# Kernel optimization log

Measured on AMD Instinct MI355X. Metric: run time of the kernel, lower is better.

Reference implementation:

```python
import jax, jax.numpy as jnp
import numpy as np
from jax import lax

NKP = 21  # hand keypoints
CH = 32   # channel width forced by K.dot(g, W) with W:[input_ch, output_dim]
OUT_DIM = 32


def setup_inputs() -> dict:
    key = jax.random.key(0)
    ks = jax.random.split(key, 9)
    B, H, W = 8, 96, 96
    s = 0.05
    return {
        "x": jax.random.normal(ks[0], (B, H, W, CH), dtype=jnp.float32),
        # shared 1x1 conv (conv2): 1x1 conv == matmul over channels
        "w2": jax.random.normal(ks[1], (CH, CH), dtype=jnp.float32) * s,
        "b2": jnp.zeros((CH,), dtype=jnp.float32),
        # per-keypoint effective 1x1 conv (conv2a over concat of identical f blocks
        # collapses exactly to a 32->32 kernel = sum of per-block slices)
        "wa": jax.random.normal(ks[2], (NKP, CH, CH), dtype=jnp.float32) * s,
        "ba": jnp.zeros((NKP, CH), dtype=jnp.float32),
        # per-keypoint 3x3 conv (conv2b), HWIO layout
        "wb": jax.random.normal(ks[3], (NKP, 3, 3, CH, CH), dtype=jnp.float32) * s,
        "bb": jnp.zeros((NKP, CH), dtype=jnp.float32),
        # per-keypoint learned projection W_i : [CH, output_dim]
        "Wp": jax.random.normal(ks[4], (NKP, CH, OUT_DIM), dtype=jnp.float32) * s,
    }


def _conv3x3(h, w, b):
    # h: [B,H,W,C], w: [3,3,C,C]
    y = lax.conv_general_dilated(h, w, (1, 1), "SAME",
                                 dimension_numbers=("NHWC", "HWIO", "NHWC"))
    return jax.nn.relu(y + b)


def reference(x, w2, b2, wa, ba, wb, bb, Wp):
    f = jax.nn.relu(jnp.einsum("bhwc,cd->bhwd", x, w2) + b2)          # [B,H,W,32]
    # per-keypoint 1x1 conv on concat([f, f_j...]) == effective 32->32 1x1 conv
    h = jax.nn.relu(jnp.einsum("bhwc,ncd->nbhwd", f, wa)
                    + ba[:, None, None, None, :])                      # [21,B,H,W,32]
    g = jax.vmap(_conv3x3)(h, wb, bb)                                  # [21,B,H,W,32]
    # sum over output_dim of (g @ W_i) == g @ W_i.sum(-1)
    lsum = jnp.einsum("nbhwc,nc->nbhw", g, Wp.sum(axis=-1))            # [21,B,H,W]
    fn = f.sum(axis=-1)[None] + lsum                                   # [21,B,H,W]
    return jnp.moveaxis(fn, 0, -1)                                     # [B,H,W,21]
```

## Files before the change

kernel.cpp:

```cpp
#include <hip/hip_runtime.h>

#define BATCH 8
#define IMH 96
#define IMW 96
#define CH 32
#define NKP 21
#define TILE 16
#define HALO 18
#define FPITCH 40
#define NPIX 324
#define NPIX_PAD 336
#define NGRP 3
#define FBLK 1152

typedef __bf16 bf16x8 __attribute__((ext_vector_type(8)));
typedef __bf16 bf16x4 __attribute__((ext_vector_type(4)));
typedef float  f32x4  __attribute__((ext_vector_type(4)));

static __device__ inline f32x4 mfma16(bf16x8 a, bf16x8 b, f32x4 c) {
    return __builtin_amdgcn_mfma_f32_16x16x32_bf16(a, b, c, 0, 0, 0);
}

__global__ void __launch_bounds__(64)
prep_kernel(const float* __restrict__ x,
            const float* __restrict__ w2, const float* __restrict__ b2,
            const float* __restrict__ wa, const float* __restrict__ wb,
            const float* __restrict__ Wp,
            __bf16* __restrict__ fout, float* __restrict__ fsum_out,
            __bf16* __restrict__ wfrag, float* __restrict__ wv)
{
    const int bx = blockIdx.x;
    const int lane = threadIdx.x;
    if (bx < FBLK) {
        const int gp = bx * 64 + lane;
        const float* xp = x + (size_t)gp * CH;
        float xv[CH];
        #pragma unroll
        for (int e = 0; e < CH; e += 4) {
            float4 v = *(const float4*)(xp + e);
            xv[e] = v.x; xv[e+1] = v.y; xv[e+2] = v.z; xv[e+3] = v.w;
        }
        float f[CH];
        #pragma unroll
        for (int c = 0; c < CH; ++c) f[c] = b2[c];
        #pragma unroll
        for (int e = 0; e < CH; ++e) {
            const float xe = xv[e];
            const float* wr = w2 + e * CH;
            #pragma unroll
            for (int c = 0; c < CH; ++c) f[c] = fmaf(xe, wr[c], f[c]);
        }
        float fs = 0.f;
        #pragma unroll
        for (int c = 0; c < CH; ++c) { f[c] = fmaxf(f[c], 0.f); fs += f[c]; }
        #pragma unroll
        for (int q = 0; q < 4; ++q) {
            bf16x8 v;
            #pragma unroll
            for (int j = 0; j < 8; ++j) v[j] = (__bf16)f[q * 8 + j];
            *(bf16x8*)&fout[(size_t)gp * CH + q * 8] = v;
        }
        fsum_out[gp] = fs;
    } else {
        const int n = bx - FBLK;
        const int r4 = lane & 15, kb = (lane >> 4) * 8;
        const float* wan = wa + n * CH * CH;
        #pragma unroll
        for (int hf = 0; hf < 2; ++hf) {
            bf16x8 v;
            #pragma unroll
            for (int j = 0; j < 8; ++j)
                v[j] = (__bf16)wan[(kb + j) * CH + hf * 16 + r4];
            *(bf16x8*)&wfrag[(((size_t)n * 20 + hf) * 64 + lane) * 8] = v;
        }
        const float* wbn = wb + (size_t)n * 9 * CH * CH;
        for (int t = 0; t < 9; ++t)
            #pragma unroll
            for (int hf = 0; hf < 2; ++hf) {
                bf16x8 v;
                #pragma unroll
                for (int j = 0; j < 8; ++j)
                    v[j] = (__bf16)wbn[(t * CH + kb + j) * CH + hf * 16 + r4];
                *(bf16x8*)&wfrag[(((size_t)n * 20 + 2 + t * 2 + hf) * 64 + lane) * 8] = v;
            }
        if (lane < CH) {
            const float* wp = Wp + (n * CH + lane) * CH;
            float s = 0.f;
            #pragma unroll
            for (int d = 0; d < CH; ++d) s += wp[d];
            wv[n * CH + lane] = s;
        }
    }
}

__global__ void __launch_bounds__(256, 4)
ckp_mfma4_kernel(const __bf16* __restrict__ fws, const float* __restrict__ fsum_ws,
                 const __bf16* __restrict__ wfrag, const float* __restrict__ wvws,
                 const float* __restrict__ ba, const float* __restrict__ bb,
                 float* __restrict__ out)
{
    __shared__ __bf16 sH[NPIX_PAD * FPITCH];

    const int tid  = threadIdx.x;
    const int tile = blockIdx.x;
    const int b    = blockIdx.y;
    const int ty0  = (tile / (IMW / TILE)) * TILE;
    const int tx0  = (tile % (IMW / TILE)) * TILE;

    const int lane = tid & 63;
    const int w    = tid >> 6;
    const int r4   = lane & 15;
    const int g16  = lane >> 4;
    const int kb   = g16 * 8;
    const int kb4  = g16 * 4;
    const int w4   = w * 4;

    int voff[6]; unsigned dmask = 0;
    #pragma unroll
    for (int i = 0; i < 6; ++i) {
        const int t  = w + 4 * i;
        const int p  = t * 16 + r4;
        const int hy = p / HALO, hx = p % HALO;
        const int Y  = ty0 + hy - 1, X = tx0 + hx - 1;
        const bool dv = (t <= 20) & (hy < HALO) & (Y >= 0) & (Y < IMH) & (X >= 0) & (X < IMW);
        const int Yc = min(max(Y, 0), IMH - 1), Xc = min(max(X, 0), IMW - 1);
        voff[i] = ((b * IMH + Yc) * IMW + Xc) * CH + kb;
        dmask |= (dv ? 1u : 0u) << i;
    }

    for (int ni = 0; ni < NGRP; ++ni) {
        const int n = blockIdx.z * NGRP + ni;
        const __bf16* wf = wfrag + (size_t)n * 20 * 64 * 8;
        bf16x8 wafr0 = *(const bf16x8*)&wf[((size_t)0 * 64 + lane) * 8];
        bf16x8 wafr1 = *(const bf16x8*)&wf[((size_t)1 * 64 + lane) * 8];
        const f32x4 ba0 = *(const f32x4*)&ba[n * CH + kb4];
        const f32x4 ba1 = *(const f32x4*)&ba[n * CH + 16 + kb4];

        if (ni) __syncthreads();

        #pragma unroll
        for (int i = 0; i < 6; ++i) {
            const int t = w + 4 * i;
            if (t <= 20) {
                bf16x8 v = *(const bf16x8*)&fws[voff[i]];
                const bool dv = (dmask >> i) & 1;
                if (!dv) {
                    #pragma unroll
                    for (int j = 0; j < 8; ++j) v[j] = (__bf16)0.f;
                }
                const f32x4 z = {0.f, 0.f, 0.f, 0.f};
                f32x4 a0 = mfma16(wafr0, v, z);
                f32x4 a1 = mfma16(wafr1, v, z);
                const int p = t * 16 + r4;
                bf16x4 h0, h1;
                #pragma unroll
                for (int r = 0; r < 4; ++r) {
                    h0[r] = dv ? (__bf16)fmaxf(a0[r] + ba0[r], 0.f) : (__bf16)0.f;
                    h1[r] = dv ? (__bf16)fmaxf(a1[r] + ba1[r], 0.f) : (__bf16)0.f;
                }
                *(bf16x4*)&sH[p * FPITCH + kb4]      = h0;
                *(bf16x4*)&sH[p * FPITCH + 16 + kb4] = h1;
            }
        }
        __syncthreads();

        f32x4 acc[4][2];
        #pragma unroll
        for (int ai = 0; ai < 4; ++ai) {
            acc[ai][0] = (f32x4){0.f, 0.f, 0.f, 0.f};
            acc[ai][1] = (f32x4){0.f, 0.f, 0.f, 0.f};
        }
        #pragma unroll
        for (int dx = 0; dx < 3; ++dx) {
            bf16x8 wt[3][2];
            #pragma unroll
            for (int dy = 0; dy < 3; ++dy)
                #pragma unroll
                for (int hf = 0; hf < 2; ++hf)
                    wt[dy][hf] = *(const bf16x8*)&wf[((size_t)(2 + (dy * 3 + dx) * 2 + hf) * 64 + lane) * 8];
            #pragma unroll
            for (int k = 0; k < 6; ++k) {
                bf16x8 hfr = *(const bf16x8*)&sH[((w4 + k) * HALO + r4 + dx) * FPITCH + kb];
                #pragma unroll
                for (int dy = 0; dy < 3; ++dy) {
                    const int ai = k - dy;
                    if (ai >= 0 && ai < 4) {
                        acc[ai][0] = mfma16(wt[dy][0], hfr, acc[ai][0]);
                        acc[ai][1] = mfma16(wt[dy][1], hfr, acc[ai][1]);
                    }
                }
            }
        }

        const f32x4 bb0 = *(const f32x4*)&bb[n * CH + kb4];
        const f32x4 bb1 = *(const f32x4*)&bb[n * CH + 16 + kb4];
        const f32x4 wv0 = *(const f32x4*)&wvws[n * CH + kb4];
        const f32x4 wv1 = *(const f32x4*)&wvws[n * CH + 16 + kb4];
        #pragma unroll
        for (int ai = 0; ai < 4; ++ai) {
            float s = 0.f;
            #pragma unroll
            for (int r = 0; r < 4; ++r) {
                s += fmaxf(acc[ai][0][r] + bb0[r], 0.f) * wv0[r];
                s += fmaxf(acc[ai][1][r] + bb1[r], 0.f) * wv1[r];
            }
            s += __shfl_xor(s, 16);
            s += __shfl_xor(s, 32);
            if (g16 == 0) {
                const int gp = (b * IMH + ty0 + w4 + ai) * IMW + tx0 + r4;
                out[(size_t)gp * NKP + n] = s + fsum_ws[gp];
            }
        }
    }
}

#define PITCH 33
__global__ void __launch_bounds__(256)
ckp_fused_kernel(const float* __restrict__ x,
                 const float* __restrict__ w2, const float* __restrict__ b2,
                 const float* __restrict__ wa, const float* __restrict__ ba,
                 const float* __restrict__ wb, const float* __restrict__ bb,
                 const float* __restrict__ Wp,
                 float* __restrict__ out)
{
    __shared__ float sH[HALO * HALO * PITCH];
    __shared__ float sFsum[TILE * TILE];
    __shared__ float sWv[CH];

    const int tid  = threadIdx.x;
    const int tile = blockIdx.x;
    const int b    = blockIdx.y;
    const int n    = blockIdx.z;
    const int ty0  = (tile / (IMW / TILE)) * TILE;
    const int tx0  = (tile % (IMW / TILE)) * TILE;

    if (tid < CH) {
        const float* wp = Wp + (n * CH + tid) * CH;
        float s = 0.f;
        #pragma unroll
        for (int d = 0; d < CH; ++d) s += wp[d];
        sWv[tid] = s;
    }
    const float* wan = wa + n * CH * CH;
    const float* ban = ba + n * CH;

    for (int p = tid; p < HALO * HALO; p += 256) {
        const int hy = p / HALO, hx = p % HALO;
        const int Y = ty0 + hy - 1, X = tx0 + hx - 1;
        float* dst = &sH[p * PITCH];
        if (Y >= 0 && Y < IMH && X >= 0 && X < IMW) {
            const float* xp = x + (((size_t)b * IMH + Y) * IMW + X) * CH;
            float xv[CH];
            #pragma unroll
            for (int e = 0; e < CH; e += 4) {
                float4 v = *(const float4*)(xp + e);
                xv[e] = v.x; xv[e+1] = v.y; xv[e+2] = v.z; xv[e+3] = v.w;
            }
            float f[CH];
            #pragma unroll
            for (int c = 0; c < CH; ++c) f[c] = b2[c];
            #pragma unroll
            for (int e = 0; e < CH; ++e) {
                const float xe = xv[e];
                const float* wr = w2 + e * CH;
                #pragma unroll
                for (int c = 0; c < CH; ++c) f[c] = fmaf(xe, wr[c], f[c]);
            }
            float fs = 0.f;
            #pragma unroll
            for (int c = 0; c < CH; ++c) { f[c] = fmaxf(f[c], 0.f); fs += f[c]; }
            if (hy >= 1 && hy <= TILE && hx >= 1 && hx <= TILE)
                sFsum[(hy - 1) * TILE + (hx - 1)] = fs;
            float h[CH];
            #pragma unroll
            for (int c = 0; c < CH; ++c) h[c] = ban[c];
            #pragma unroll
            for (int e = 0; e < CH; ++e) {
                const float fe = f[e];
                const float* wr = wan + e * CH;
                #pragma unroll
                for (int c = 0; c < CH; ++c) h[c] = fmaf(fe, wr[c], h[c]);
            }
            #pragma unroll
            for (int c = 0; c < CH; ++c) dst[c] = fmaxf(h[c], 0.f);
        } else {
            #pragma unroll
            for (int c = 0; c < CH; ++c) dst[c] = 0.f;
        }
    }
    __syncthreads();

    const int iy = tid / TILE, ix = tid % TILE;
    const float* wbn = wb + n * 9 * CH * CH;
    const float* bbn = bb + n * CH;
    float g[CH];
    #pragma unroll
    for (int c = 0; c < CH; ++c) g[c] = bbn[c];
    for (int dy = 0; dy < 3; ++dy) {
        for (int dx = 0; dx < 3; ++dx) {
            const float* hrow = &sH[((iy + dy) * HALO + (ix + dx)) * PITCH];
            const float* wr0 = wbn + (dy * 3 + dx) * CH * CH;
            #pragma unroll
            for (int e = 0; e < CH; ++e) {
                const float hv = hrow[e];
                const float* wr = wr0 + e * CH;
                #pragma unroll
                for (int c = 0; c < CH; ++c) g[c] = fmaf(hv, wr[c], g[c]);
            }
        }
    }
    float lsum = 0.f;
    #pragma unroll
    for (int c = 0; c < CH; ++c) lsum = fmaf(fmaxf(g[c], 0.f), sWv[c], lsum);
    const int Y = ty0 + iy, X = tx0 + ix;
    out[(((size_t)b * IMH + Y) * IMW + X) * NKP + n] = sFsum[tid] + lsum;
}

extern "C" void kernel_launch(void* const* d_in, const int* in_sizes, int n_in,
                              void* d_out, int out_size, void* d_ws, size_t ws_size,
                              hipStream_t stream) {
    const float* x  = (const float*)d_in[0];
    const float* w2 = (const float*)d_in[1];
    const float* b2 = (const float*)d_in[2];
    const float* wa = (const float*)d_in[3];
    const float* ba = (const float*)d_in[4];
    const float* wb = (const float*)d_in[5];
    const float* bb = (const float*)d_in[6];
    const float* Wp = (const float*)d_in[7];
    float* out = (float*)d_out;

    const size_t npix     = (size_t)BATCH * IMH * IMW;
    const size_t f_bytes  = npix * CH * sizeof(__bf16);
    const size_t fs_bytes = npix * sizeof(float);
    const size_t wf_bytes = (size_t)NKP * 20 * 64 * 8 * sizeof(__bf16);
    const size_t wv_bytes = (size_t)NKP * CH * sizeof(float);
    const size_t need = f_bytes + fs_bytes + wf_bytes + wv_bytes;

    if (ws_size >= need) {
        __bf16* f_ws    = (__bf16*)d_ws;
        float*  fsum_ws = (float*)((char*)d_ws + f_bytes);
        __bf16* wf_ws   = (__bf16*)((char*)d_ws + f_bytes + fs_bytes);
        float*  wv_ws   = (float*)((char*)d_ws + f_bytes + fs_bytes + wf_bytes);

        prep_kernel<<<dim3(FBLK + NKP), dim3(64), 0, stream>>>(
            x, w2, b2, wa, wb, Wp, f_ws, fsum_ws, wf_ws, wv_ws);
        dim3 grid((IMH / TILE) * (IMW / TILE), BATCH, NKP / NGRP);
        ckp_mfma4_kernel<<<grid, dim3(256), 0, stream>>>(f_ws, fsum_ws, wf_ws, wv_ws, ba, bb, out);
    } else {
        dim3 grid((IMH / TILE) * (IMW / TILE), BATCH, NKP);
        ckp_fused_kernel<<<grid, dim3(256), 0, stream>>>(x, w2, b2, wa, ba, wb, bb, Wp, out);
    }
}
```

Before: 54.42 us.

## Assign one keypoint per block and loop over two tiles with register-resident weights

The main conv kernel now gives each block a single keypoint and walks two spatial tiles, instead of one tile and three keypoints. All 3x3 weight fragments and biases are loaded into registers once per block, and the feature loads for a tile are issued together before the MFMA stage. This cuts repeated weight fetches and makes loads more independent, but it raises register pressure, so launch bounds drop to 3 blocks per CU. The grid becomes 18x8x21 blocks.

After: 89.41 us. 64.3% more time.

```diff
diff --git a/kernel.cpp b/kernel.cpp
--- a/kernel.cpp
+++ b/kernel.cpp
@@ -10,8 +10,8 @@
 #define FPITCH 40
 #define NPIX 324
 #define NPIX_PAD 336
-#define NGRP 3
 #define FBLK 1152
+#define NTP 2
 
 typedef __bf16 bf16x8 __attribute__((ext_vector_type(8)));
 typedef __bf16 bf16x4 __attribute__((ext_vector_type(4)));
@@ -93,19 +93,18 @@
     }
 }
 
-__global__ void __launch_bounds__(256, 4)
-ckp_mfma4_kernel(const __bf16* __restrict__ fws, const float* __restrict__ fsum_ws,
+__global__ void __launch_bounds__(256, 3)
+ckp_mfma5_kernel(const __bf16* __restrict__ fws, const float* __restrict__ fsum_ws,
                  const __bf16* __restrict__ wfrag, const float* __restrict__ wvws,
                  const float* __restrict__ ba, const float* __restrict__ bb,
                  float* __restrict__ out)
 {
     __shared__ __bf16 sH[NPIX_PAD * FPITCH];
 
-    const int tid  = threadIdx.x;
-    const int tile = blockIdx.x;
-    const int b    = blockIdx.y;
-    const int ty0  = (tile / (IMW / TILE)) * TILE;
-    const int tx0  = (tile % (IMW / TILE)) * TILE;
+    const int tid = threadIdx.x;
+    const int gx  = blockIdx.x;
+    const int b   = blockIdx.y;
+    const int n   = blockIdx.z;
 
     const int lane = tid & 63;
     const int w    = tid >> 6;
@@ -115,34 +114,51 @@
     const int kb4  = g16 * 4;
     const int w4   = w * 4;
 
-    int voff[6]; unsigned dmask = 0;
+    const __bf16* wf = wfrag + (size_t)n * 20 * 64 * 8;
+    const bf16x8 wafr0 = *(const bf16x8*)&wf[((size_t)0 * 64 + lane) * 8];
+    const bf16x8 wafr1 = *(const bf16x8*)&wf[((size_t)1 * 64 + lane) * 8];
+    bf16x8 wtfr[9][2];
     #pragma unroll
-    for (int i = 0; i < 6; ++i) {
-        const int t  = w + 4 * i;
-        const int p  = t * 16 + r4;
-        const int hy = p / HALO, hx = p % HALO;
-        const int Y  = ty0 + hy - 1, X = tx0 + hx - 1;
-        const bool dv = (t <= 20) & (hy < HALO) & (Y >= 0) & (Y < IMH) & (X >= 0) & (X < IMW);
-        const int Yc = min(max(Y, 0), IMH - 1), Xc = min(max(X, 0), IMW - 1);
-        voff[i] = ((b * IMH + Yc) * IMW + Xc) * CH + kb;
-        dmask |= (dv ? 1u : 0u) << i;
-    }
-
-    for (int ni = 0; ni < NGRP; ++ni) {
-        const int n = blockIdx.z * NGRP + ni;
-        const __bf16* wf = wfrag + (size_t)n * 20 * 64 * 8;
-        bf16x8 wafr0 = *(const bf16x8*)&wf[((size_t)0 * 64 + lane) * 8];
-        bf16x8 wafr1 = *(const bf16x8*)&wf[((size_t)1 * 64 + lane) * 8];
-        const f32x4 ba0 = *(const f32x4*)&ba[n * CH + kb4];
-        const f32x4 ba1 = *(const f32x4*)&ba[n * CH + 16 + kb4];
-
-        if (ni) __syncthreads();
-
+    for (int t = 0; t < 9; ++t)
+        #pragma unroll
+        for (int hf = 0; hf < 2; ++hf)
+            wtfr[t][hf] = *(const bf16x8*)&wf[((size_t)(2 + t * 2 + hf) * 64 + lane) * 8];
+    const f32x4 ba0 = *(const f32x4*)&ba[n * CH + kb4];
+    const f32x4 ba1 = *(const f32x4*)&ba[n * CH + 16 + kb4];
+    const f32x4 bb0 = *(const f32x4*)&bb[n * CH + kb4];
+    const f32x4 bb1 = *(const f32x4*)&bb[n * CH + 16 + kb4];
+    const f32x4 wv0 = *(const f32x4*)&wvws[n * CH + kb4];
+    const f32x4 wv1 = *(const f32x4*)&wvws[n * CH + 16 + kb4];
+
+    for (int tp = 0; tp < NTP; ++tp) {
+        const int tile = gx * NTP + tp;
+        const int ty0  = (tile / (IMW / TILE)) * TILE;
+        const int tx0  = (tile % (IMW / TILE)) * TILE;
+
+        int voff[6]; unsigned dmask = 0;
+        #pragma unroll
+        for (int i = 0; i < 6; ++i) {
+            const int t  = w + 4 * i;
+            const int p  = t * 16 + r4;
+            const int hy = p / HALO, hx = p % HALO;
+            const int Y  = ty0 + hy - 1, X = tx0 + hx - 1;
+            const bool dv = (t <= 20) & (hy < HALO) & (Y >= 0) & (Y < IMH) & (X >= 0) & (X < IMW);
+            const int Yc = min(max(Y, 0), IMH - 1), Xc = min(max(X, 0), IMW - 1);
+            voff[i] = ((b * IMH + Yc) * IMW + Xc) * CH + kb;
+            dmask |= (dv ? 1u : 0u) << i;
+        }
+
+        if (tp) __syncthreads();
+
+        bf16x8 fv[6];
+        #pragma unroll
+        for (int i = 0; i < 6; ++i)
+            fv[i] = *(const bf16x8*)&fws[voff[i]];
         #pragma unroll
         for (int i = 0; i < 6; ++i) {
             const int t = w + 4 * i;
             if (t <= 20) {
-                bf16x8 v = *(const bf16x8*)&fws[voff[i]];
+                bf16x8 v = fv[i];
                 const bool dv = (dmask >> i) & 1;
                 if (!dv) {
                     #pragma unroll
@@ -172,12 +188,6 @@
         }
         #pragma unroll
         for (int dx = 0; dx < 3; ++dx) {
-            bf16x8 wt[3][2];
-            #pragma unroll
-            for (int dy = 0; dy < 3; ++dy)
-                #pragma unroll
-                for (int hf = 0; hf < 2; ++hf)
-                    wt[dy][hf] = *(const bf16x8*)&wf[((size_t)(2 + (dy * 3 + dx) * 2 + hf) * 64 + lane) * 8];
             #pragma unroll
             for (int k = 0; k < 6; ++k) {
                 bf16x8 hfr = *(const bf16x8*)&sH[((w4 + k) * HALO + r4 + dx) * FPITCH + kb];
@@ -185,17 +195,13 @@
                 for (int dy = 0; dy < 3; ++dy) {
                     const int ai = k - dy;
                     if (ai >= 0 && ai < 4) {
-                        acc[ai][0] = mfma16(wt[dy][0], hfr, acc[ai][0]);
-                        acc[ai][1] = mfma16(wt[dy][1], hfr, acc[ai][1]);
+                        acc[ai][0] = mfma16(wtfr[dy * 3 + dx][0], hfr, acc[ai][0]);
+                        acc[ai][1] = mfma16(wtfr[dy * 3 + dx][1], hfr, acc[ai][1]);
                     }
                 }
             }
         }
 
-        const f32x4 bb0 = *(const f32x4*)&bb[n * CH + kb4];
-        const f32x4 bb1 = *(const f32x4*)&bb[n * CH + 16 + kb4];
-        const f32x4 wv0 = *(const f32x4*)&wvws[n * CH + kb4];
-        const f32x4 wv1 = *(const f32x4*)&wvws[n * CH + 16 + kb4];
         #pragma unroll
         for (int ai = 0; ai < 4; ++ai) {
             float s = 0.f;
@@ -344,8 +350,8 @@
 
         prep_kernel<<<dim3(FBLK + NKP), dim3(64), 0, stream>>>(
             x, w2, b2, wa, wb, Wp, f_ws, fsum_ws, wf_ws, wv_ws);
-        dim3 grid((IMH / TILE) * (IMW / TILE), BATCH, NKP / NGRP);
-        ckp_mfma4_kernel<<<grid, dim3(256), 0, stream>>>(f_ws, fsum_ws, wf_ws, wv_ws, ba, bb, out);
+        dim3 grid((IMH / TILE) * (IMW / TILE) / NTP, BATCH, NKP);
+        ckp_mfma5_kernel<<<grid, dim3(256), 0, stream>>>(f_ws, fsum_ws, wf_ws, wv_ws, ba, bb, out);
     } else {
         dim3 grid((IMH / TILE) * (IMW / TILE), BATCH, NKP);
         ckp_fused_kernel<<<grid, dim3(256), 0, stream>>>(x, w2, b2, wa, ba, wb, bb, Wp, out);
```

## Software-pipeline keypoint loop with double-buffered LDS and hoisted feature loads

Applied to the files above, without the earlier changes.

Restructures the per-keypoint loop into a skewed software pipeline. The 1x1 conv for keypoint n+1 writes into one of two LDS buffers while the 3x3 conv for keypoint n reads the other, which cuts one barrier per iteration. The halo feature vectors and fsum values are now loaded once into registers before the loop rather than reloaded for every keypoint, and the biases are folded into the MFMA accumulator init. In exchange, LDS use doubles and register pressure rises, so the occupancy hint drops from 4 to 2 blocks per CU.

New measurement: 55.65 us. 2.3% more time.

```diff
diff --git a/kernel.cpp b/kernel.cpp
--- a/kernel.cpp
+++ b/kernel.cpp
@@ -93,19 +93,20 @@
     }
 }
 
-__global__ void __launch_bounds__(256, 4)
-ckp_mfma4_kernel(const __bf16* __restrict__ fws, const float* __restrict__ fsum_ws,
+__global__ void __launch_bounds__(256, 2)
+ckp_mfma6_kernel(const __bf16* __restrict__ fws, const float* __restrict__ fsum_ws,
                  const __bf16* __restrict__ wfrag, const float* __restrict__ wvws,
                  const float* __restrict__ ba, const float* __restrict__ bb,
                  float* __restrict__ out)
 {
-    __shared__ __bf16 sH[NPIX_PAD * FPITCH];
-
-    const int tid  = threadIdx.x;
-    const int tile = blockIdx.x;
-    const int b    = blockIdx.y;
-    const int ty0  = (tile / (IMW / TILE)) * TILE;
-    const int tx0  = (tile % (IMW / TILE)) * TILE;
+    __shared__ __bf16 sH[2][NPIX_PAD * FPITCH];
+
+    const int tid   = threadIdx.x;
+    const int tile  = blockIdx.x;
+    const int b     = blockIdx.y;
+    const int nbase = blockIdx.z * NGRP;
+    const int ty0   = (tile / (IMW / TILE)) * TILE;
+    const int tx0   = (tile % (IMW / TILE)) * TILE;
 
     const int lane = tid & 63;
     const int w    = tid >> 6;
@@ -115,7 +116,7 @@
     const int kb4  = g16 * 4;
     const int w4   = w * 4;
 
-    int voff[6]; unsigned dmask = 0;
+    bf16x8 fv[6]; unsigned dmask = 0;
     #pragma unroll
     for (int i = 0; i < 6; ++i) {
         const int t  = w + 4 * i;
@@ -124,93 +125,103 @@
         const int Y  = ty0 + hy - 1, X = tx0 + hx - 1;
         const bool dv = (t <= 20) & (hy < HALO) & (Y >= 0) & (Y < IMH) & (X >= 0) & (X < IMW);
         const int Yc = min(max(Y, 0), IMH - 1), Xc = min(max(X, 0), IMW - 1);
-        voff[i] = ((b * IMH + Yc) * IMW + Xc) * CH + kb;
+        bf16x8 v = *(const bf16x8*)&fws[((b * IMH + Yc) * IMW + Xc) * CH + kb];
+        if (!dv) {
+            #pragma unroll
+            for (int j = 0; j < 8; ++j) v[j] = (__bf16)0.f;
+        }
+        fv[i] = v;
         dmask |= (dv ? 1u : 0u) << i;
     }
-
-    for (int ni = 0; ni < NGRP; ++ni) {
-        const int n = blockIdx.z * NGRP + ni;
-        const __bf16* wf = wfrag + (size_t)n * 20 * 64 * 8;
-        bf16x8 wafr0 = *(const bf16x8*)&wf[((size_t)0 * 64 + lane) * 8];
-        bf16x8 wafr1 = *(const bf16x8*)&wf[((size_t)1 * 64 + lane) * 8];
-        const f32x4 ba0 = *(const f32x4*)&ba[n * CH + kb4];
-        const f32x4 ba1 = *(const f32x4*)&ba[n * CH + 16 + kb4];
-
-        if (ni) __syncthreads();
-
-        #pragma unroll
-        for (int i = 0; i < 6; ++i) {
-            const int t = w + 4 * i;
-            if (t <= 20) {
-                bf16x8 v = *(const bf16x8*)&fws[voff[i]];
-                const bool dv = (dmask >> i) & 1;
-                if (!dv) {
+    float fs4[4];
+    #pragma unroll
+    for (int ai = 0; ai < 4; ++ai)
+        fs4[ai] = fsum_ws[(b * IMH + ty0 + w4 + ai) * IMW + tx0 + r4];
+
+    #pragma unroll
+    for (int ni = 0; ni <= NGRP; ++ni) {
+        if (ni < NGRP) {
+            const int n = nbase + ni;
+            const __bf16* wf = wfrag + (size_t)n * 20 * 64 * 8;
+            const bf16x8 wafr0 = *(const bf16x8*)&wf[((size_t)0 * 64 + lane) * 8];
+            const bf16x8 wafr1 = *(const bf16x8*)&wf[((size_t)1 * 64 + lane) * 8];
+            const f32x4 ba0 = *(const f32x4*)&ba[n * CH + kb4];
+            const f32x4 ba1 = *(const f32x4*)&ba[n * CH + 16 + kb4];
+            __bf16* sb = &sH[ni & 1][0];
+            #pragma unroll
+            for (int i = 0; i < 6; ++i) {
+                const int t = w + 4 * i;
+                if (t <= 20) {
+                    f32x4 a0 = mfma16(wafr0, fv[i], ba0);
+                    f32x4 a1 = mfma16(wafr1, fv[i], ba1);
+                    const int p = t * 16 + r4;
+                    const bool dv = (dmask >> i) & 1;
+                    bf16x4 h0, h1;
                     #pragma unroll
-                    for (int j = 0; j < 8; ++j) v[j] = (__bf16)0.f;
+                    for (int r = 0; r < 4; ++r) {
+                        h0[r] = dv ? (__bf16)fmaxf(a0[r], 0.f) : (__bf16)0.f;
+                        h1[r] = dv ? (__bf16)fmaxf(a1[r], 0.f) : (__bf16)0.f;
+                    }
+                    *(bf16x4*)&sb[p * FPITCH + kb4]      = h0;
+                    *(bf16x4*)&sb[p * FPITCH + 16 + kb4] = h1;
                 }
-                const f32x4 z = {0.f, 0.f, 0.f, 0.f};
-                f32x4 a0 = mfma16(wafr0, v, z);
-                f32x4 a1 = mfma16(wafr1, v, z);
-                const int p = t * 16 + r4;
-                bf16x4 h0, h1;
-                #pragma unroll
-                for (int r = 0; r < 4; ++r) {
-                    h0[r] = dv ? (__bf16)fmaxf(a0[r] + ba0[r], 0.f) : (__bf16)0.f;
-                    h1[r] = dv ? (__bf16)fmaxf(a1[r] + ba1[r], 0.f) : (__bf16)0.f;
-                }
-                *(bf16x4*)&sH[p * FPITCH + kb4]      = h0;
-                *(bf16x4*)&sH[p * FPITCH + 16 + kb4] = h1;
-            }
-        }
-        __syncthreads();
-
-        f32x4 acc[4][2];
-        #pragma unroll
-        for (int ai = 0; ai < 4; ++ai) {
-            acc[ai][0] = (f32x4){0.f, 0.f, 0.f, 0.f};
-            acc[ai][1] = (f32x4){0.f, 0.f, 0.f, 0.f};
-        }
-        #pragma unroll
-        for (int dx = 0; dx < 3; ++dx) {
-            bf16x8 wt[3][2];
-            #pragma unroll
-            for (int dy = 0; dy < 3; ++dy)
-                #pragma unroll
-                for (int hf = 0; hf < 2; ++hf)
-                    wt[dy][hf] = *(const bf16x8*)&wf[((size_t)(2 + (dy * 3 + dx) * 2 + hf) * 64 + lane) * 8];
-            #pragma unroll
-            for (int k = 0; k < 6; ++k) {
-                bf16x8 hfr = *(const bf16x8*)&sH[((w4 + k) * HALO + r4 + dx) * FPITCH + kb];
-                #pragma unroll
-                for (int dy = 0; dy < 3; ++dy) {
-                    const int ai = k - dy;
-                    if (ai >= 0 && ai < 4) {
-                        acc[ai][0] = mfma16(wt[dy][0], hfr, acc[ai][0]);
-                        acc[ai][1] = mfma16(wt[dy][1], hfr, acc[ai][1]);
+            }
+        }
+
+        if (ni > 0) {
+            const int n = nbase + ni - 1;
+            const __bf16* wf = wfrag + (size_t)n * 20 * 64 * 8;
+            const f32x4 bb0 = *(const f32x4*)&bb[n * CH + kb4];
+            const f32x4 bb1 = *(const f32x4*)&bb[n * CH + 16 + kb4];
+            const f32x4 wv0 = *(const f32x4*)&wvws[n * CH + kb4];
+            const f32x4 wv1 = *(const f32x4*)&wvws[n * CH + 16 + kb4];
+            const __bf16* sb = &sH[(ni - 1) & 1][0];
+
+            f32x4 acc[4][2];
+            #pragma unroll
+            for (int ai = 0; ai < 4; ++ai) {
+                acc[ai][0] = bb0;
+                acc[ai][1] = bb1;
+            }
+            #pragma unroll
+            for (int dx = 0; dx < 3; ++dx) {
+                bf16x8 wt[3][2];
+                #pragma unroll
+                for (int dy = 0; dy < 3; ++dy)
+                    #pragma unroll
+                    for (int hf = 0; hf < 2; ++hf)
+                        wt[dy][hf] = *(const bf16x8*)&wf[((size_t)(2 + (dy * 3 + dx) * 2 + hf) * 64 + lane) * 8];
+                #pragma unroll
+                for (int k = 0; k < 6; ++k) {
+                    bf16x8 hfr = *(const bf16x8*)&sb[((w4 + k) * HALO + r4 + dx) * FPITCH + kb];
+                    #pragma unroll
+                    for (int dy = 0; dy < 3; ++dy) {
+                        const int ai = k - dy;
+                        if (ai >= 0 && ai < 4) {
+                            acc[ai][0] = mfma16(wt[dy][0], hfr, acc[ai][0]);
+                            acc[ai][1] = mfma16(wt[dy][1], hfr, acc[ai][1]);
+                        }
                     }
                 }
             }
-        }
-
-        const f32x4 bb0 = *(const f32x4*)&bb[n * CH + kb4];
-        const f32x4 bb1 = *(const f32x4*)&bb[n * CH + 16 + kb4];
-        const f32x4 wv0 = *(const f32x4*)&wvws[n * CH + kb4];
-        const f32x4 wv1 = *(const f32x4*)&wvws[n * CH + 16 + kb4];
-        #pragma unroll
-        for (int ai = 0; ai < 4; ++ai) {
-            float s = 0.f;
-            #pragma unroll
-            for (int r = 0; r < 4; ++r) {
-                s += fmaxf(acc[ai][0][r] + bb0[r], 0.f) * wv0[r];
-                s += fmaxf(acc[ai][1][r] + bb1[r], 0.f) * wv1[r];
-            }
-            s += __shfl_xor(s, 16);
-            s += __shfl_xor(s, 32);
-            if (g16 == 0) {
-                const int gp = (b * IMH + ty0 + w4 + ai) * IMW + tx0 + r4;
-                out[(size_t)gp * NKP + n] = s + fsum_ws[gp];
-            }
-        }
+            #pragma unroll
+            for (int ai = 0; ai < 4; ++ai) {
+                float s = 0.f;
+                #pragma unroll
+                for (int r = 0; r < 4; ++r) {
+                    s += fmaxf(acc[ai][0][r], 0.f) * wv0[r];
+                    s += fmaxf(acc[ai][1][r], 0.f) * wv1[r];
+                }
+                s += __shfl_xor(s, 16);
+                s += __shfl_xor(s, 32);
+                if (g16 == 0) {
+                    const int gp = (b * IMH + ty0 + w4 + ai) * IMW + tx0 + r4;
+                    out[(size_t)gp * NKP + n] = s + fs4[ai];
+                }
+            }
+        }
+
+        if (ni < NGRP) __syncthreads();
     }
 }
 
@@ -345,7 +356,7 @@
         prep_kernel<<<dim3(FBLK + NKP), dim3(64), 0, stream>>>(
             x, w2, b2, wa, wb, Wp, f_ws, fsum_ws, wf_ws, wv_ws);
         dim3 grid((IMH / TILE) * (IMW / TILE), BATCH, NKP / NGRP);
-        ckp_mfma4_kernel<<<grid, dim3(256), 0, stream>>>(f_ws, fsum_ws, wf_ws, wv_ws, ba, bb, out);
+        ckp_mfma6_kernel<<<grid, dim3(256), 0, stream>>>(f_ws, fsum_ws, wf_ws, wv_ws, ba, bb, out);
     } else {
         dim3 grid((IMH / TILE) * (IMW / TILE), BATCH, NKP);
         ckp_fused_kernel<<<grid, dim3(256), 0, stream>>>(x, w2, b2, wa, ba, wb, bb, Wp, out);
```

## Switch conv kernel to 32x32x16 MFMA with 32x8 tiles and folded biases

Applied to the files above, without the earlier changes.

Replaces the 16x16x32 bf16 MFMA path with 32x32x16 MFMA and rebuilds the weight fragment layout in the prep kernel to match. The spatial tile changes from 16x16 to 32-wide by 8-tall, so each wave covers two full 32-pixel rows with a 34x10 halo. Biases are now loaded as accumulator fragments, removing separate bias adds, and the reduction shuffles drop from two to one. The goal is fewer MFMA issues and less LDS and shuffle traffic per output. The cost is a larger halo overhead per tile and a different LDS access pattern that could cause bank conflicts.

Measured after the change: 63.53 us (median of 2 runs). 16.7% more time.

```diff
diff --git a/kernel.cpp b/kernel.cpp
--- a/kernel.cpp
+++ b/kernel.cpp
@@ -5,20 +5,24 @@
 #define IMW 96
 #define CH 32
 #define NKP 21
-#define TILE 16
-#define HALO 18
+#define TW 32
+#define TH 8
+#define HW 34
+#define HH 10
+#define NPIXH 340
+#define NSTRIP 11
+#define NSLOT 352
 #define FPITCH 40
-#define NPIX 324
-#define NPIX_PAD 336
 #define NGRP 3
 #define FBLK 1152
 
 typedef __bf16 bf16x8 __attribute__((ext_vector_type(8)));
 typedef __bf16 bf16x4 __attribute__((ext_vector_type(4)));
 typedef float  f32x4  __attribute__((ext_vector_type(4)));
-
-static __device__ inline f32x4 mfma16(bf16x8 a, bf16x8 b, f32x4 c) {
-    return __builtin_amdgcn_mfma_f32_16x16x32_bf16(a, b, c, 0, 0, 0);
+typedef float  f32x16 __attribute__((ext_vector_type(16)));
+
+static __device__ inline f32x16 mfma32(bf16x8 a, bf16x8 b, f32x16 c) {
+    return __builtin_amdgcn_mfma_f32_32x32x16_bf16(a, b, c, 0, 0, 0);
 }
 
 __global__ void __launch_bounds__(64)
@@ -63,25 +67,25 @@
         fsum_out[gp] = fs;
     } else {
         const int n = bx - FBLK;
-        const int r4 = lane & 15, kb = (lane >> 4) * 8;
+        const int m = lane & 31, hi = lane >> 5;
         const float* wan = wa + n * CH * CH;
         #pragma unroll
-        for (int hf = 0; hf < 2; ++hf) {
+        for (int kh = 0; kh < 2; ++kh) {
             bf16x8 v;
             #pragma unroll
             for (int j = 0; j < 8; ++j)
-                v[j] = (__bf16)wan[(kb + j) * CH + hf * 16 + r4];
-            *(bf16x8*)&wfrag[(((size_t)n * 20 + hf) * 64 + lane) * 8] = v;
+                v[j] = (__bf16)wan[(kh * 16 + hi * 8 + j) * CH + m];
+            *(bf16x8*)&wfrag[(((size_t)n * 20 + kh) * 64 + lane) * 8] = v;
         }
         const float* wbn = wb + (size_t)n * 9 * CH * CH;
         for (int t = 0; t < 9; ++t)
             #pragma unroll
-            for (int hf = 0; hf < 2; ++hf) {
+            for (int kh = 0; kh < 2; ++kh) {
                 bf16x8 v;
                 #pragma unroll
                 for (int j = 0; j < 8; ++j)
-                    v[j] = (__bf16)wbn[(t * CH + kb + j) * CH + hf * 16 + r4];
-                *(bf16x8*)&wfrag[(((size_t)n * 20 + 2 + t * 2 + hf) * 64 + lane) * 8] = v;
+                    v[j] = (__bf16)wbn[(t * CH + kh * 16 + hi * 8 + j) * CH + m];
+                *(bf16x8*)&wfrag[(((size_t)n * 20 + 2 + t * 2 + kh) * 64 + lane) * 8] = v;
             }
         if (lane < CH) {
             const float* wp = Wp + (n * CH + lane) * CH;
@@ -93,128 +97,142 @@
     }
 }
 
+static __device__ inline f32x16 load_cfrag(const float* p, int hi) {
+    f32x16 out;
+    #pragma unroll
+    for (int q = 0; q < 4; ++q) {
+        f32x4 v = *(const f32x4*)&p[q * 8 + hi * 4];
+        #pragma unroll
+        for (int r = 0; r < 4; ++r) out[q * 4 + r] = v[r];
+    }
+    return out;
+}
+
 __global__ void __launch_bounds__(256, 4)
-ckp_mfma4_kernel(const __bf16* __restrict__ fws, const float* __restrict__ fsum_ws,
+ckp_mfma7_kernel(const __bf16* __restrict__ fws, const float* __restrict__ fsum_ws,
                  const __bf16* __restrict__ wfrag, const float* __restrict__ wvws,
                  const float* __restrict__ ba, const float* __restrict__ bb,
                  float* __restrict__ out)
 {
-    __shared__ __bf16 sH[NPIX_PAD * FPITCH];
-
-    const int tid  = threadIdx.x;
-    const int tile = blockIdx.x;
-    const int b    = blockIdx.y;
-    const int ty0  = (tile / (IMW / TILE)) * TILE;
-    const int tx0  = (tile % (IMW / TILE)) * TILE;
+    __shared__ __bf16 sH[NSLOT * FPITCH];
+
+    const int tid   = threadIdx.x;
+    const int tile  = blockIdx.x;
+    const int b     = blockIdx.y;
+    const int nbase = blockIdx.z * NGRP;
+    const int ty0   = (tile % (IMH / TH)) * TH;
+    const int tx0   = (tile / (IMH / TH)) * TW;
 
     const int lane = tid & 63;
     const int w    = tid >> 6;
-    const int r4   = lane & 15;
-    const int g16  = lane >> 4;
-    const int kb   = g16 * 8;
-    const int kb4  = g16 * 4;
-    const int w4   = w * 4;
-
-    int voff[6]; unsigned dmask = 0;
-    #pragma unroll
-    for (int i = 0; i < 6; ++i) {
+    const int c5   = lane & 31;
+    const int hi   = lane >> 5;
+    const int w2r  = w * 2;
+
+    int voff[3]; unsigned dmask = 0;
+    #pragma unroll
+    for (int i = 0; i < 3; ++i) {
         const int t  = w + 4 * i;
-        const int p  = t * 16 + r4;
-        const int hy = p / HALO, hx = p % HALO;
+        const int px = t * 32 + c5;
+        const int hy = px / HW, hx = px % HW;
         const int Y  = ty0 + hy - 1, X = tx0 + hx - 1;
-        const bool dv = (t <= 20) & (hy < HALO) & (Y >= 0) & (Y < IMH) & (X >= 0) & (X < IMW);
+        const bool dv = (px < NPIXH) & (Y >= 0) & (Y < IMH) & (X >= 0) & (X < IMW);
         const int Yc = min(max(Y, 0), IMH - 1), Xc = min(max(X, 0), IMW - 1);
-        voff[i] = ((b * IMH + Yc) * IMW + Xc) * CH + kb;
+        voff[i] = ((b * IMH + Yc) * IMW + Xc) * CH + hi * 8;
         dmask |= (dv ? 1u : 0u) << i;
     }
+    int wo[3];
+    #pragma unroll
+    for (int i = 0; i < 3; ++i) wo[i] = ((w + 4 * i) * 32 + c5) * FPITCH + 4 * hi;
+    int ro[4];
+    #pragma unroll
+    for (int h4 = 0; h4 < 4; ++h4) ro[h4] = ((w2r + h4) * HW + c5) * FPITCH + 8 * hi;
+    float fs2[2];
+    #pragma unroll
+    for (int ri = 0; ri < 2; ++ri)
+        fs2[ri] = fsum_ws[(b * IMH + ty0 + w2r + ri) * IMW + tx0 + c5];
 
     for (int ni = 0; ni < NGRP; ++ni) {
-        const int n = blockIdx.z * NGRP + ni;
+        const int n = nbase + ni;
         const __bf16* wf = wfrag + (size_t)n * 20 * 64 * 8;
-        bf16x8 wafr0 = *(const bf16x8*)&wf[((size_t)0 * 64 + lane) * 8];
-        bf16x8 wafr1 = *(const bf16x8*)&wf[((size_t)1 * 64 + lane) * 8];
-        const f32x4 ba0 = *(const f32x4*)&ba[n * CH + kb4];
-        const f32x4 ba1 = *(const f32x4*)&ba[n * CH + 16 + kb4];
+        const bf16x8 wa0 = *(const bf16x8*)&wf[((size_t)0 * 64 + lane) * 8];
+        const bf16x8 wa1 = *(const bf16x8*)&wf[((size_t)1 * 64 + lane) * 8];
+        const f32x16 baf = load_cfrag(ba + n * CH, hi);
 
         if (ni) __syncthreads();
 
         #pragma unroll
-        for (int i = 0; i < 6; ++i) {
+        for (int i = 0; i < 3; ++i) {
             const int t = w + 4 * i;
-            if (t <= 20) {
-                bf16x8 v = *(const bf16x8*)&fws[voff[i]];
+            if (t < NSTRIP) {
+                bf16x8 f0 = *(const bf16x8*)&fws[voff[i]];
+                bf16x8 f1 = *(const bf16x8*)&fws[voff[i] + 16];
+                f32x16 a = mfma32(wa0, f0, baf);
+                a = mfma32(wa1, f1, a);
                 const bool dv = (dmask >> i) & 1;
-                if (!dv) {
+                #pragma unroll
+                for (int q = 0; q < 4; ++q) {
+                    bf16x4 hq;
                     #pragma unroll
-                    for (int j = 0; j < 8; ++j) v[j] = (__bf16)0.f;
+                    for (int r = 0; r < 4; ++r)
+                        hq[r] = dv ? (__bf16)fmaxf(a[q * 4 + r], 0.f) : (__bf16)0.f;
+                    *(bf16x4*)&sH[wo[i] + 8 * q] = hq;
                 }
-                const f32x4 z = {0.f, 0.f, 0.f, 0.f};
-                f32x4 a0 = mfma16(wafr0, v, z);
-                f32x4 a1 = mfma16(wafr1, v, z);
-                const int p = t * 16 + r4;
-                bf16x4 h0, h1;
-                #pragma unroll
-                for (int r = 0; r < 4; ++r) {
-                    h0[r] = dv ? (__bf16)fmaxf(a0[r] + ba0[r], 0.f) : (__bf16)0.f;
-                    h1[r] = dv ? (__bf16)fmaxf(a1[r] + ba1[r], 0.f) : (__bf16)0.f;
-                }
-                *(bf16x4*)&sH[p * FPITCH + kb4]      = h0;
-                *(bf16x4*)&sH[p * FPITCH + 16 + kb4] = h1;
             }
         }
         __syncthreads();
 
-        f32x4 acc[4][2];
-        #pragma unroll
-        for (int ai = 0; ai < 4; ++ai) {
-            acc[ai][0] = (f32x4){0.f, 0.f, 0.f, 0.f};
-            acc[ai][1] = (f32x4){0.f, 0.f, 0.f, 0.f};
-        }
+        const f32x16 bbf = load_cfrag(bb + n * CH, hi);
+        f32x16 acc0, acc1;
         #pragma unroll
         for (int dx = 0; dx < 3; ++dx) {
             bf16x8 wt[3][2];
             #pragma unroll
             for (int dy = 0; dy < 3; ++dy)
                 #pragma unroll
-                for (int hf = 0; hf < 2; ++hf)
-                    wt[dy][hf] = *(const bf16x8*)&wf[((size_t)(2 + (dy * 3 + dx) * 2 + hf) * 64 + lane) * 8];
-            #pragma unroll
-            for (int k = 0; k < 6; ++k) {
-                bf16x8 hfr = *(const bf16x8*)&sH[((w4 + k) * HALO + r4 + dx) * FPITCH + kb];
+                for (int kh = 0; kh < 2; ++kh)
+                    wt[dy][kh] = *(const bf16x8*)&wf[((size_t)(2 + (dy * 3 + dx) * 2 + kh) * 64 + lane) * 8];
+            #pragma unroll
+            for (int h4 = 0; h4 < 4; ++h4) {
+                const int ad = ro[h4] + dx * FPITCH;
+                bf16x8 B0 = *(const bf16x8*)&sH[ad];
+                bf16x8 B1 = *(const bf16x8*)&sH[ad + 16];
                 #pragma unroll
                 for (int dy = 0; dy < 3; ++dy) {
-                    const int ai = k - dy;
-                    if (ai >= 0 && ai < 4) {
-                        acc[ai][0] = mfma16(wt[dy][0], hfr, acc[ai][0]);
-                        acc[ai][1] = mfma16(wt[dy][1], hfr, acc[ai][1]);
+                    const int ri = h4 - dy;
+                    if (ri == 0) {
+                        const bool first = (dx == 0 && dy == 0);
+                        acc0 = mfma32(wt[dy][0], B0, first ? bbf : acc0);
+                        acc0 = mfma32(wt[dy][1], B1, acc0);
+                    } else if (ri == 1) {
+                        const bool first = (dx == 0 && dy == 0);
+                        acc1 = mfma32(wt[dy][0], B0, first ? bbf : acc1);
+                        acc1 = mfma32(wt[dy][1], B1, acc1);
                     }
                 }
             }
         }
 
-        const f32x4 bb0 = *(const f32x4*)&bb[n * CH + kb4];
-        const f32x4 bb1 = *(const f32x4*)&bb[n * CH + 16 + kb4];
-        const f32x4 wv0 = *(const f32x4*)&wvws[n * CH + kb4];
-        const f32x4 wv1 = *(const f32x4*)&wvws[n * CH + 16 + kb4];
-        #pragma unroll
-        for (int ai = 0; ai < 4; ++ai) {
+        const f32x16 wvf = load_cfrag(wvws + n * CH, hi);
+        #pragma unroll
+        for (int ri = 0; ri < 2; ++ri) {
+            const f32x16 acc = ri ? acc1 : acc0;
             float s = 0.f;
             #pragma unroll
-            for (int r = 0; r < 4; ++r) {
-                s += fmaxf(acc[ai][0][r] + bb0[r], 0.f) * wv0[r];
-                s += fmaxf(acc[ai][1][r] + bb1[r], 0.f) * wv1[r];
-            }
-            s += __shfl_xor(s, 16);
+            for (int r = 0; r < 16; ++r)
+                s += fmaxf(acc[r], 0.f) * wvf[r];
             s += __shfl_xor(s, 32);
-            if (g16 == 0) {
-                const int gp = (b * IMH + ty0 + w4 + ai) * IMW + tx0 + r4;
-                out[(size_t)gp * NKP + n] = s + fsum_ws[gp];
+            if (hi == 0) {
+                const int gp = (b * IMH + ty0 + w2r + ri) * IMW + tx0 + c5;
+                out[(size_t)gp * NKP + n] = s + fs2[ri];
             }
         }
     }
 }
 
 #define PITCH 33
+#define FTILE 16
+#define FHALO 18
 __global__ void __launch_bounds__(256)
 ckp_fused_kernel(const float* __restrict__ x,
                  const float* __restrict__ w2, const float* __restrict__ b2,
@@ -223,16 +241,16 @@
                  const float* __restrict__ Wp,
                  float* __restrict__ out)
 {
-    __shared__ float sH[HALO * HALO * PITCH];
-    __shared__ float sFsum[TILE * TILE];
+    __shared__ float sH[FHALO * FHALO * PITCH];
+    __shared__ float sFsum[FTILE * FTILE];
     __shared__ float sWv[CH];
 
     const int tid  = threadIdx.x;
     const int tile = blockIdx.x;
     const int b    = blockIdx.y;
     const int n    = blockIdx.z;
-    const int ty0  = (tile / (IMW / TILE)) * TILE;
-    const int tx0  = (tile % (IMW / TILE)) * TILE;
+    const int ty0  = (tile / (IMW / FTILE)) * FTILE;
+    const int tx0  = (tile % (IMW / FTILE)) * FTILE;
 
     if (tid < CH) {
         const float* wp = Wp + (n * CH + tid) * CH;
@@ -244,8 +262,8 @@
     const float* wan = wa + n * CH * CH;
     const float* ban = ba + n * CH;
 
-    for (int p = tid; p < HALO * HALO; p += 256) {
-        const int hy = p / HALO, hx = p % HALO;
+    for (int p = tid; p < FHALO * FHALO; p += 256) {
+        const int hy = p / FHALO, hx = p % FHALO;
         const int Y = ty0 + hy - 1, X = tx0 + hx - 1;
         float* dst = &sH[p * PITCH];
         if (Y >= 0 && Y < IMH && X >= 0 && X < IMW) {
@@ -269,8 +287,8 @@
             float fs = 0.f;
             #pragma unroll
             for (int c = 0; c < CH; ++c) { f[c] = fmaxf(f[c], 0.f); fs += f[c]; }
-            if (hy >= 1 && hy <= TILE && hx >= 1 && hx <= TILE)
-                sFsum[(hy - 1) * TILE + (hx - 1)] = fs;
+            if (hy >= 1 && hy <= FTILE && hx >= 1 && hx <= FTILE)
+                sFsum[(hy - 1) * FTILE + (hx - 1)] = fs;
             float h[CH];
             #pragma unroll
             for (int c = 0; c < CH; ++c) h[c] = ban[c];
@@ -290,7 +308,7 @@
     }
     __syncthreads();
 
-    const int iy = tid / TILE, ix = tid % TILE;
+    const int iy = tid / FTILE, ix = tid % FTILE;
     const float* wbn = wb + n * 9 * CH * CH;
     const float* bbn = bb + n * CH;
     float g[CH];
@@ -298,7 +316,7 @@
     for (int c = 0; c < CH; ++c) g[c] = bbn[c];
     for (int dy = 0; dy < 3; ++dy) {
         for (int dx = 0; dx < 3; ++dx) {
-            const float* hrow = &sH[((iy + dy) * HALO + (ix + dx)) * PITCH];
+            const float* hrow = &sH[((iy + dy) * FHALO + (ix + dx)) * PITCH];
             const float* wr0 = wbn + (dy * 3 + dx) * CH * CH;
             #pragma unroll
             for (int e = 0; e < CH; ++e) {
@@ -344,10 +362,10 @@
 
         prep_kernel<<<dim3(FBLK + NKP), dim3(64), 0, stream>>>(
             x, w2, b2, wa, wb, Wp, f_ws, fsum_ws, wf_ws, wv_ws);
-        dim3 grid((IMH / TILE) * (IMW / TILE), BATCH, NKP / NGRP);
-        ckp_mfma4_kernel<<<grid, dim3(256), 0, stream>>>(f_ws, fsum_ws, wf_ws, wv_ws, ba, bb, out);
+        dim3 grid((IMW / TW) * (IMH / TH), BATCH, NKP / NGRP);
+        ckp_mfma7_kernel<<<grid, dim3(256), 0, stream>>>(f_ws, fsum_ws, wf_ws, wv_ws, ba, bb, out);
     } else {
-        dim3 grid((IMH / TILE) * (IMW / TILE), BATCH, NKP);
+        dim3 grid((IMW / FTILE) * (IMH / FTILE), BATCH, NKP);
         ckp_fused_kernel<<<grid, dim3(256), 0, stream>>>(x, w2, b2, wa, ba, wb, bb, Wp, out);
     }
 }
```
